# Kernel optimization log

Hardware: AMD Instinct MI355X
Metric: run time of the kernel (lower is better)

## Reference

```python
import jax, jax.numpy as jnp
import numpy as np

B = 16384      # batch
D_IN = 512     # layer_channels[0]
D = 1024       # hidden width (layer_channels[1..4])
R = 16         # num_relations
SCALE = 0.02


def setup_inputs() -> dict:
    key = jax.random.key(0)
    ks = jax.random.split(key, 8)
    return {
        "x": jax.random.normal(ks[0], (B, D_IN), dtype=jnp.float32),
        "relations": jax.random.randint(ks[1], (B,), 0, R, dtype=jnp.int32),
        # non-relation dense stack (2 layers)
        "W0": jax.random.normal(ks[2], (D_IN, D), dtype=jnp.float32) * SCALE,
        "b0": jnp.zeros((D,), dtype=jnp.float32),
        "W1": jax.random.normal(ks[3], (D, D), dtype=jnp.float32) * SCALE,
        "b1": jnp.zeros((D,), dtype=jnp.float32),
        # relation-aware layers (3 layers due to the module's range(i, num_layers))
        "RW1": jax.random.normal(ks[4], (R, D, D), dtype=jnp.float32) * SCALE,
        "Rb1": jnp.zeros((R, D), dtype=jnp.float32),
        "RW2": jax.random.normal(ks[5], (R, D, D), dtype=jnp.float32) * SCALE,
        "Rb2": jnp.zeros((R, D), dtype=jnp.float32),
        "RW3": jax.random.normal(ks[6], (R, D, D), dtype=jnp.float32) * SCALE,
        "Rb3": jnp.zeros((R, D), dtype=jnp.float32),
    }


def _relation_linear(h, W, b, relations):
    """Per-sample weight selection: out[n] = h[n] @ W[rel[n]] + b[rel[n]].
    Computed as R masked GEMMs to avoid materializing per-sample [B,D,D] weights.
    """
    out = jnp.zeros((h.shape[0], W.shape[2]), dtype=h.dtype)
    for r in range(W.shape[0]):  # fixed small expert set -> ok to unroll
        mask = (relations == r)[:, None]
        out = out + jnp.where(mask, h @ W[r] + b[r], jnp.zeros((), h.dtype))
    return out


def reference(x, relations, W0, b0, W1, b1, RW1, Rb1, RW2, Rb2, RW3, Rb3):
    # non_relation_pred: Linear -> ReLU -> (dropout=identity), twice
    h = jax.nn.relu(x @ W0 + b0)
    h = jax.nn.relu(h @ W1 + b1)
    # relation layers: relu+dropout between, none after last; bn disabled
    h = jax.nn.relu(_relation_linear(h, RW1, Rb1, relations))
    h = jax.nn.relu(_relation_linear(h, RW2, Rb2, relations))
    h = _relation_linear(h, RW3, Rb3, relations)
    return h
```

## Files before the change

kernel.cpp:

```cpp
#include <hip/hip_runtime.h>
#include <stdint.h>

#define B_ROWS   16384
#define D_IN     512
#define N_DIM    1024
#define NREL     16
#define TM       128
#define TN       128
#define BK       32
#define MAX_TILES 144
#define PADDED_ROWS (MAX_TILES * TM)

typedef __bf16 bf16x8 __attribute__((ext_vector_type(8)));
typedef float  f32x4  __attribute__((ext_vector_type(4)));

__device__ __forceinline__ uint16_t f2bf(float f) {
  union { float f; uint32_t u; } v; v.f = f;
  return (uint16_t)((v.u + 0x7fffu + ((v.u >> 16) & 1u)) >> 16);
}

__device__ __forceinline__ void async_cp16(const uint16_t* g, uint16_t* l) {
  __builtin_amdgcn_global_load_lds(
      (__attribute__((address_space(1))) void*)(g),
      (__attribute__((address_space(3))) void*)(l), 16, 0, 0);
}

__global__ void setup_kernel(const int* __restrict__ rel, int* __restrict__ rowidx,
                             int* __restrict__ texp, int* __restrict__ tval) {
  __shared__ int cnt[NREL], segstart[NREL], cursor[NREL];
  const int t = threadIdx.x;
  if (t < NREL) { cnt[t] = 0; cursor[t] = 0; }
  __syncthreads();
  for (int i = t; i < B_ROWS; i += 256) atomicAdd(&cnt[rel[i]], 1);
  __syncthreads();
  if (t == 0) {
    int slot = 0, tile = 0;
    for (int r = 0; r < NREL; r++) {
      segstart[r] = slot;
      const int c = cnt[r];
      const int nt = (c + TM - 1) / TM;
      for (int k = 0; k < nt; k++) {
        texp[tile + k] = r;
        const int rem = c - k * TM;
        tval[tile + k] = rem < TM ? rem : TM;
      }
      tile += nt; slot += nt * TM;
    }
    for (; tile < MAX_TILES; tile++) { texp[tile] = 0; tval[tile] = 0; }
  }
  __syncthreads();
  for (int i = t; i < PADDED_ROWS; i += 256) rowidx[i] = 0;
  __syncthreads();
  for (int i = t; i < B_ROWS; i += 256) {
    const int r = rel[i];
    const int p = atomicAdd(&cursor[r], 1);
    rowidx[segstart[r] + p] = i;
  }
}

__global__ void conv_x_kernel(const float* __restrict__ in, uint16_t* __restrict__ out, int n4) {
  const int i = blockIdx.x * blockDim.x + threadIdx.x;
  if (i < n4) {
    const float4 v = ((const float4*)in)[i];
    uint2 o;
    o.x = (uint32_t)f2bf(v.x) | ((uint32_t)f2bf(v.y) << 16);
    o.y = (uint32_t)f2bf(v.z) | ((uint32_t)f2bf(v.w) << 16);
    ((uint2*)out)[i] = o;
  }
}

__global__ void transpose_conv_kernel(const float* __restrict__ W, uint16_t* __restrict__ Wt,
                                      int K, int N) {
  __shared__ uint16_t tile[32][33];
  const size_t mat = (size_t)K * N;
  const float*    Wp  = W  + mat * blockIdx.z;
  uint16_t*       Wtp = Wt + mat * blockIdx.z;
  const int n0 = blockIdx.x * 32, k0 = blockIdx.y * 32;
  const int tx = threadIdx.x & 31, ty = threadIdx.x >> 5;
  #pragma unroll
  for (int kk = ty; kk < 32; kk += 8)
    tile[kk][tx] = f2bf(Wp[(size_t)(k0 + kk) * N + n0 + tx]);
  __syncthreads();
  #pragma unroll
  for (int nn = ty; nn < 32; nn += 8)
    Wtp[(size_t)(n0 + nn) * K + k0 + tx] = tile[tx][nn];
}

template<bool GATHER, bool EXPERT, bool RELU, bool SCATTER>
__global__ __launch_bounds__(256)
void gemm_kernel(const uint16_t* __restrict__ A, const uint16_t* __restrict__ W,
                 const float* __restrict__ bias, void* __restrict__ outp,
                 const int* __restrict__ rowidx, const int* __restrict__ texp,
                 const int* __restrict__ tval, int K) {
  __shared__ uint16_t sA[TM * BK];
  __shared__ uint16_t sB[TN * BK];

  const int tid = threadIdx.x;
  const int w = tid >> 6, l = tid & 63;
  const int m0 = blockIdx.y * TM;
  const int n0 = blockIdx.x * TN;

  int e = 0, valid = TM;
  if (EXPERT) {
    e = texp[blockIdx.y];
    valid = tval[blockIdx.y];
    if (valid == 0) return;
  }

  const int lrow0 = 16 * w + (l >> 2);
  const int lrow1 = 64 + lrow0;
  const int koff  = (l & 3) * 8;
  int ar0 = m0 + lrow0, ar1 = m0 + lrow1;
  if (GATHER) { ar0 = rowidx[ar0]; ar1 = rowidx[ar1]; }
  const uint16_t* srcA0 = A + (size_t)ar0 * K + koff;
  const uint16_t* srcA1 = A + (size_t)ar1 * K + koff;
  const uint16_t* Wb    = W + (size_t)e * N_DIM * K;
  const uint16_t* srcB0 = Wb + (size_t)(n0 + lrow0) * K + koff;
  const uint16_t* srcB1 = Wb + (size_t)(n0 + lrow1) * K + koff;
  uint16_t* ldsA0 = &sA[w * 512 + l * 8];
  uint16_t* ldsA1 = &sA[2048 + w * 512 + l * 8];
  uint16_t* ldsB0 = &sB[w * 512 + l * 8];
  uint16_t* ldsB1 = &sB[2048 + w * 512 + l * 8];

  const int wm = w >> 1, wn = w & 1;
  const int q = l >> 4, r16 = l & 15;

  f32x4 acc[4][4];
  #pragma unroll
  for (int i = 0; i < 4; i++)
    #pragma unroll
    for (int j = 0; j < 4; j++) {
      f32x4 z = {0.f, 0.f, 0.f, 0.f};
      acc[i][j] = z;
    }

  for (int k0 = 0; k0 < K; k0 += BK) {
    async_cp16(srcA0 + k0, ldsA0);
    async_cp16(srcA1 + k0, ldsA1);
    async_cp16(srcB0 + k0, ldsB0);
    async_cp16(srcB1 + k0, ldsB1);
    __syncthreads();
    bf16x8 af[4], bf[4];
    #pragma unroll
    for (int i = 0; i < 4; i++) {
      af[i] = *(const bf16x8*)(&sA[(wm * 64 + i * 16 + r16) * BK + q * 8]);
      bf[i] = *(const bf16x8*)(&sB[(wn * 64 + i * 16 + r16) * BK + q * 8]);
    }
    #pragma unroll
    for (int i = 0; i < 4; i++)
      #pragma unroll
      for (int j = 0; j < 4; j++)
        acc[i][j] = __builtin_amdgcn_mfma_f32_16x16x32_bf16(af[i], bf[j], acc[i][j], 0, 0, 0);
    __syncthreads();
  }

  float bj[4];
  #pragma unroll
  for (int j = 0; j < 4; j++)
    bj[j] = bias[(size_t)e * N_DIM + n0 + wn * 64 + j * 16 + r16];

  #pragma unroll
  for (int i = 0; i < 4; i++) {
    #pragma unroll
    for (int r = 0; r < 4; r++) {
      const int rl = wm * 64 + i * 16 + q * 4 + r;
      if (SCATTER) {
        if (rl < valid) {
          const int orow = rowidx[m0 + rl];
          float* o = (float*)outp + (size_t)orow * N_DIM + n0 + wn * 64 + r16;
          #pragma unroll
          for (int j = 0; j < 4; j++) {
            float v = acc[i][j][r] + bj[j];
            if (RELU) v = fmaxf(v, 0.f);
            o[j * 16] = v;
          }
        }
      } else {
        uint16_t* o = (uint16_t*)outp + (size_t)(m0 + rl) * N_DIM + n0 + wn * 64 + r16;
        #pragma unroll
        for (int j = 0; j < 4; j++) {
          float v = acc[i][j][r] + bj[j];
          if (RELU) v = fmaxf(v, 0.f);
          o[j * 16] = f2bf(v);
        }
      }
    }
  }
}

extern "C" void kernel_launch(void* const* d_in, const int* in_sizes, int n_in,
                              void* d_out, int out_size, void* d_ws, size_t ws_size,
                              hipStream_t stream) {
  const float* x   = (const float*)d_in[0];
  const int*   rel = (const int*)d_in[1];
  const float* W0  = (const float*)d_in[2];
  const float* b0  = (const float*)d_in[3];
  const float* W1  = (const float*)d_in[4];
  const float* b1  = (const float*)d_in[5];
  const float* RW1 = (const float*)d_in[6];
  const float* Rb1 = (const float*)d_in[7];
  const float* RW2 = (const float*)d_in[8];
  const float* Rb2 = (const float*)d_in[9];
  const float* RW3 = (const float*)d_in[10];
  const float* Rb3 = (const float*)d_in[11];
  float* out = (float*)d_out;

  char* ws = (char*)d_ws;
  uint16_t* xb = (uint16_t*)(ws);
  uint16_t* wt = (uint16_t*)(ws + (size_t)(16u << 20));
  uint16_t* ha = (uint16_t*)(ws + (size_t)(48u << 20));
  uint16_t* hb = (uint16_t*)(ws + (size_t)(84u << 20));
  int* rowidx = (int*)(ws + (size_t)(120u << 20));
  int* texp   = rowidx + PADDED_ROWS;
  int* tval   = texp + MAX_TILES;

  const dim3 blk(256);
  const dim3 gDense(N_DIM / TN, B_ROWS / TM);
  const dim3 gRel(N_DIM / TN, MAX_TILES);

  setup_kernel<<<dim3(1), blk, 0, stream>>>(rel, rowidx, texp, tval);
  conv_x_kernel<<<dim3((B_ROWS * D_IN) / 4 / 256), blk, 0, stream>>>(x, xb, (B_ROWS * D_IN) / 4);

  transpose_conv_kernel<<<dim3(N_DIM / 32, D_IN / 32, 1), blk, 0, stream>>>(W0, wt, D_IN, N_DIM);
  gemm_kernel<false, false, true, false><<<gDense, blk, 0, stream>>>(
      xb, wt, b0, ha, nullptr, nullptr, nullptr, D_IN);

  transpose_conv_kernel<<<dim3(N_DIM / 32, N_DIM / 32, 1), blk, 0, stream>>>(W1, wt, N_DIM, N_DIM);
  gemm_kernel<false, false, true, false><<<gDense, blk, 0, stream>>>(
      ha, wt, b1, hb, nullptr, nullptr, nullptr, N_DIM);

  transpose_conv_kernel<<<dim3(N_DIM / 32, N_DIM / 32, NREL), blk, 0, stream>>>(RW1, wt, N_DIM, N_DIM);
  gemm_kernel<true, true, true, false><<<gRel, blk, 0, stream>>>(
      hb, wt, Rb1, ha, rowidx, texp, tval, N_DIM);

  transpose_conv_kernel<<<dim3(N_DIM / 32, N_DIM / 32, NREL), blk, 0, stream>>>(RW2, wt, N_DIM, N_DIM);
  gemm_kernel<false, true, true, false><<<gRel, blk, 0, stream>>>(
      ha, wt, Rb2, hb, rowidx, texp, tval, N_DIM);

  transpose_conv_kernel<<<dim3(N_DIM / 32, N_DIM / 32, NREL), blk, 0, stream>>>(RW3, wt, N_DIM, N_DIM);
  gemm_kernel<false, true, false, true><<<gRel, blk, 0, stream>>>(
      hb, wt, Rb3, out, rowidx, texp, tval, N_DIM);

  (void)in_sizes; (void)n_in; (void)out_size; (void)ws_size;
}
```

Measured before the change: 633.5 us.

## Swizzle LDS tiles, remap blocks per XCD, vectorize weight transpose

Three changes at once. The GEMM now applies an XOR swizzle to the LDS k-chunk layout to cut bank conflicts on the fragment reads. It also launches a 1D grid remapped so each XCD handles contiguous M rows, which should improve L2 reuse. The weight transpose-convert kernel moves to 64x64 tiles with float4 loads and packed bf16 pair stores. The new block mapping assumes a grid size that is a multiple of 64 with 8 N-tiles, so it is tied to these fixed dimensions.

```diff
diff --git a/kernel.cpp b/kernel.cpp
--- a/kernel.cpp
+++ b/kernel.cpp
@@ -69,21 +69,34 @@
   }
 }
 
-__global__ void transpose_conv_kernel(const float* __restrict__ W, uint16_t* __restrict__ Wt,
-                                      int K, int N) {
-  __shared__ uint16_t tile[32][33];
+__global__ __launch_bounds__(256)
+void transpose_conv_kernel(const float* __restrict__ W, uint16_t* __restrict__ Wt,
+                           int K, int N) {
+  __shared__ uint32_t t32[64][33];
   const size_t mat = (size_t)K * N;
   const float*    Wp  = W  + mat * blockIdx.z;
   uint16_t*       Wtp = Wt + mat * blockIdx.z;
-  const int n0 = blockIdx.x * 32, k0 = blockIdx.y * 32;
-  const int tx = threadIdx.x & 31, ty = threadIdx.x >> 5;
-  #pragma unroll
-  for (int kk = ty; kk < 32; kk += 8)
-    tile[kk][tx] = f2bf(Wp[(size_t)(k0 + kk) * N + n0 + tx]);
-  __syncthreads();
-  #pragma unroll
-  for (int nn = ty; nn < 32; nn += 8)
-    Wtp[(size_t)(n0 + nn) * K + k0 + tx] = tile[tx][nn];
+  const int n0 = blockIdx.x * 64, k0 = blockIdx.y * 64;
+  const int tx = threadIdx.x & 15;
+  const int ty = threadIdx.x >> 4;
+  #pragma unroll
+  for (int rb = 0; rb < 2; rb++) {
+    const int kp = rb * 16 + ty;
+    const int k  = k0 + kp * 2;
+    const float4 r0 = *(const float4*)&Wp[(size_t)k * N + n0 + tx * 4];
+    const float4 r1 = *(const float4*)&Wp[(size_t)(k + 1) * N + n0 + tx * 4];
+    t32[tx * 4 + 0][kp] = (uint32_t)f2bf(r0.x) | ((uint32_t)f2bf(r1.x) << 16);
+    t32[tx * 4 + 1][kp] = (uint32_t)f2bf(r0.y) | ((uint32_t)f2bf(r1.y) << 16);
+    t32[tx * 4 + 2][kp] = (uint32_t)f2bf(r0.z) | ((uint32_t)f2bf(r1.z) << 16);
+    t32[tx * 4 + 3][kp] = (uint32_t)f2bf(r0.w) | ((uint32_t)f2bf(r1.w) << 16);
+  }
+  __syncthreads();
+  #pragma unroll
+  for (int rb = 0; rb < 4; rb++) {
+    const int nl = rb * 16 + ty;
+    uint2 v; v.x = t32[nl][2 * tx]; v.y = t32[nl][2 * tx + 1];
+    *(uint2*)&Wtp[(size_t)(n0 + nl) * K + k0 + tx * 4] = v;
+  }
 }
 
 template<bool GATHER, bool EXPERT, bool RELU, bool SCATTER>
@@ -97,26 +110,34 @@
 
   const int tid = threadIdx.x;
   const int w = tid >> 6, l = tid & 63;
-  const int m0 = blockIdx.y * TM;
-  const int n0 = blockIdx.x * TN;
+
+  const int lin = blockIdx.x;
+  const int xcd = lin & 7;
+  const int j   = lin >> 3;
+  const int mpx = gridDim.x >> 6;
+  const int my  = xcd * mpx + (j >> 3);
+  const int nx  = j & 7;
+  const int m0 = my * TM;
+  const int n0 = nx * TN;
 
   int e = 0, valid = TM;
   if (EXPERT) {
-    e = texp[blockIdx.y];
-    valid = tval[blockIdx.y];
+    e = texp[my];
+    valid = tval[my];
     if (valid == 0) return;
   }
 
-  const int lrow0 = 16 * w + (l >> 2);
-  const int lrow1 = 64 + lrow0;
-  const int koff  = (l & 3) * 8;
-  int ar0 = m0 + lrow0, ar1 = m0 + lrow1;
+  const int lrow16 = l >> 2;
+  const int row0   = 16 * w + lrow16;
+  const int sel    = (row0 ^ (row0 >> 2)) & 3;
+  const int koff   = ((l & 3) ^ sel) * 8;
+  int ar0 = m0 + row0, ar1 = m0 + 64 + row0;
   if (GATHER) { ar0 = rowidx[ar0]; ar1 = rowidx[ar1]; }
   const uint16_t* srcA0 = A + (size_t)ar0 * K + koff;
   const uint16_t* srcA1 = A + (size_t)ar1 * K + koff;
   const uint16_t* Wb    = W + (size_t)e * N_DIM * K;
-  const uint16_t* srcB0 = Wb + (size_t)(n0 + lrow0) * K + koff;
-  const uint16_t* srcB1 = Wb + (size_t)(n0 + lrow1) * K + koff;
+  const uint16_t* srcB0 = Wb + (size_t)(n0 + row0) * K + koff;
+  const uint16_t* srcB1 = Wb + (size_t)(n0 + 64 + row0) * K + koff;
   uint16_t* ldsA0 = &sA[w * 512 + l * 8];
   uint16_t* ldsA1 = &sA[2048 + w * 512 + l * 8];
   uint16_t* ldsB0 = &sB[w * 512 + l * 8];
@@ -124,14 +145,15 @@
 
   const int wm = w >> 1, wn = w & 1;
   const int q = l >> 4, r16 = l & 15;
+  const int selr = (r16 ^ (r16 >> 2)) & 3;
 
   f32x4 acc[4][4];
   #pragma unroll
   for (int i = 0; i < 4; i++)
     #pragma unroll
-    for (int j = 0; j < 4; j++) {
+    for (int jj = 0; jj < 4; jj++) {
       f32x4 z = {0.f, 0.f, 0.f, 0.f};
-      acc[i][j] = z;
+      acc[i][jj] = z;
     }
 
   for (int k0 = 0; k0 < K; k0 += BK) {
@@ -141,23 +163,24 @@
     async_cp16(srcB1 + k0, ldsB1);
     __syncthreads();
     bf16x8 af[4], bf[4];
+    const int cq = (q ^ selr) * 8;
     #pragma unroll
     for (int i = 0; i < 4; i++) {
-      af[i] = *(const bf16x8*)(&sA[(wm * 64 + i * 16 + r16) * BK + q * 8]);
-      bf[i] = *(const bf16x8*)(&sB[(wn * 64 + i * 16 + r16) * BK + q * 8]);
+      af[i] = *(const bf16x8*)(&sA[(wm * 64 + i * 16 + r16) * BK + cq]);
+      bf[i] = *(const bf16x8*)(&sB[(wn * 64 + i * 16 + r16) * BK + cq]);
     }
     #pragma unroll
     for (int i = 0; i < 4; i++)
       #pragma unroll
-      for (int j = 0; j < 4; j++)
-        acc[i][j] = __builtin_amdgcn_mfma_f32_16x16x32_bf16(af[i], bf[j], acc[i][j], 0, 0, 0);
+      for (int jj = 0; jj < 4; jj++)
+        acc[i][jj] = __builtin_amdgcn_mfma_f32_16x16x32_bf16(af[i], bf[jj], acc[i][jj], 0, 0, 0);
     __syncthreads();
   }
 
   float bj[4];
   #pragma unroll
-  for (int j = 0; j < 4; j++)
-    bj[j] = bias[(size_t)e * N_DIM + n0 + wn * 64 + j * 16 + r16];
+  for (int jj = 0; jj < 4; jj++)
+    bj[jj] = bias[(size_t)e * N_DIM + n0 + wn * 64 + jj * 16 + r16];
 
   #pragma unroll
   for (int i = 0; i < 4; i++) {
@@ -169,19 +192,19 @@
           const int orow = rowidx[m0 + rl];
           float* o = (float*)outp + (size_t)orow * N_DIM + n0 + wn * 64 + r16;
           #pragma unroll
-          for (int j = 0; j < 4; j++) {
-            float v = acc[i][j][r] + bj[j];
+          for (int jj = 0; jj < 4; jj++) {
+            float v = acc[i][jj][r] + bj[jj];
             if (RELU) v = fmaxf(v, 0.f);
-            o[j * 16] = v;
+            o[jj * 16] = v;
           }
         }
       } else {
         uint16_t* o = (uint16_t*)outp + (size_t)(m0 + rl) * N_DIM + n0 + wn * 64 + r16;
         #pragma unroll
-        for (int j = 0; j < 4; j++) {
-          float v = acc[i][j][r] + bj[j];
+        for (int jj = 0; jj < 4; jj++) {
+          float v = acc[i][jj][r] + bj[jj];
           if (RELU) v = fmaxf(v, 0.f);
-          o[j * 16] = f2bf(v);
+          o[jj * 16] = f2bf(v);
         }
       }
     }
@@ -215,29 +238,29 @@
   int* tval   = texp + MAX_TILES;
 
   const dim3 blk(256);
-  const dim3 gDense(N_DIM / TN, B_ROWS / TM);
-  const dim3 gRel(N_DIM / TN, MAX_TILES);
+  const dim3 gDense(8 * (B_ROWS / TM));
+  const dim3 gRel(8 * MAX_TILES);
 
   setup_kernel<<<dim3(1), blk, 0, stream>>>(rel, rowidx, texp, tval);
   conv_x_kernel<<<dim3((B_ROWS * D_IN) / 4 / 256), blk, 0, stream>>>(x, xb, (B_ROWS * D_IN) / 4);
 
-  transpose_conv_kernel<<<dim3(N_DIM / 32, D_IN / 32, 1), blk, 0, stream>>>(W0, wt, D_IN, N_DIM);
+  transpose_conv_kernel<<<dim3(N_DIM / 64, D_IN / 64, 1), blk, 0, stream>>>(W0, wt, D_IN, N_DIM);
   gemm_kernel<false, false, true, false><<<gDense, blk, 0, stream>>>(
       xb, wt, b0, ha, nullptr, nullptr, nullptr, D_IN);
 
-  transpose_conv_kernel<<<dim3(N_DIM / 32, N_DIM / 32, 1), blk, 0, stream>>>(W1, wt, N_DIM, N_DIM);
+  transpose_conv_kernel<<<dim3(N_DIM / 64, N_DIM / 64, 1), blk, 0, stream>>>(W1, wt, N_DIM, N_DIM);
   gemm_kernel<false, false, true, false><<<gDense, blk, 0, stream>>>(
       ha, wt, b1, hb, nullptr, nullptr, nullptr, N_DIM);
 
-  transpose_conv_kernel<<<dim3(N_DIM / 32, N_DIM / 32, NREL), blk, 0, stream>>>(RW1, wt, N_DIM, N_DIM);
+  transpose_conv_kernel<<<dim3(N_DIM / 64, N_DIM / 64, NREL), blk, 0, stream>>>(RW1, wt, N_DIM, N_DIM);
   gemm_kernel<true, true, true, false><<<gRel, blk, 0, stream>>>(
       hb, wt, Rb1, ha, rowidx, texp, tval, N_DIM);
 
-  transpose_conv_kernel<<<dim3(N_DIM / 32, N_DIM / 32, NREL), blk, 0, stream>>>(RW2, wt, N_DIM, N_DIM);
+  transpose_conv_kernel<<<dim3(N_DIM / 64, N_DIM / 64, NREL), blk, 0, stream>>>(RW2, wt, N_DIM, N_DIM);
   gemm_kernel<false, true, true, false><<<gRel, blk, 0, stream>>>(
       ha, wt, Rb2, hb, rowidx, texp, tval, N_DIM);
 
-  transpose_conv_kernel<<<dim3(N_DIM / 32, N_DIM / 32, NREL), blk, 0, stream>>>(RW3, wt, N_DIM, N_DIM);
+  transpose_conv_kernel<<<dim3(N_DIM / 64, N_DIM / 64, NREL), blk, 0, stream>>>(RW3, wt, N_DIM, N_DIM);
   gemm_kernel<false, true, false, true><<<gRel, blk, 0, stream>>>(
       hb, wt, Rb3, out, rowidx, texp, tval, N_DIM);
 
```

Result: faster. 574.2 us (-9.4%).
